# Kernel tuning notes

Measured on AMD Instinct MI355X. Metric: run time of the kernel, lower is better.

Reference implementation:

```python
import jax, jax.numpy as jnp
import numpy as np

D = 1024
H = 8  # num_heads hardcoded in module
B = 16384


def setup_inputs() -> dict:
    key = jax.random.key(0)
    ks = jax.random.split(key, 12)
    s = 0.02
    return {
        "text_feat": jax.random.normal(ks[0], (B, D), jnp.float32),
        "image_feat": jax.random.normal(ks[1], (B, D), jnp.float32),
        # fuse_proj (nn.Linear): y = x @ W.T + b
        "fuse_w": jax.random.normal(ks[2], (D, D), jnp.float32) * s,
        "fuse_b": jax.random.normal(ks[3], (D,), jnp.float32) * s,
        # text_to_fused MHA params (torch packed in_proj layout: [Wq;Wk;Wv])
        "t_in_w": jax.random.normal(ks[4], (3 * D, D), jnp.float32) * s,
        "t_in_b": jax.random.normal(ks[5], (3 * D,), jnp.float32) * s,
        "t_out_w": jax.random.normal(ks[6], (D, D), jnp.float32) * s,
        "t_out_b": jax.random.normal(ks[7], (D,), jnp.float32) * s,
        # image_to_fused MHA params
        "i_in_w": jax.random.normal(ks[8], (3 * D, D), jnp.float32) * s,
        "i_in_b": jax.random.normal(ks[9], (3 * D,), jnp.float32) * s,
        "i_out_w": jax.random.normal(ks[10], (D, D), jnp.float32) * s,
        "i_out_b": jax.random.normal(ks[11], (D,), jnp.float32) * s,
    }


def _mha_len1(q_feat, kv_feat, in_w, in_b, out_w, out_b):
    """nn.MultiheadAttention with query/key/value of seq-len 1 (eval, no dropout)."""
    d = q_feat.shape[-1]
    dh = d // H
    wq, wk, wv = in_w[:d], in_w[d:2 * d], in_w[2 * d:]
    bq, bk, bv = in_b[:d], in_b[d:2 * d], in_b[2 * d:]
    q = (q_feat @ wq.T + bq).reshape(-1, H, dh)   # (B,H,dh)
    k = (kv_feat @ wk.T + bk).reshape(-1, H, dh)
    v = (kv_feat @ wv.T + bv).reshape(-1, H, dh)
    scores = jnp.sum(q * k, axis=-1) / jnp.sqrt(jnp.asarray(dh, q.dtype))  # (B,H)
    attn = jax.nn.softmax(scores[..., None], axis=-1)  # (B,H,1) -> all ones
    o = (attn * v).reshape(-1, d)                  # (B,D)
    return o @ out_w.T + out_b


def reference(text_feat, image_feat, fuse_w, fuse_b,
              t_in_w, t_in_b, t_out_w, t_out_b,
              i_in_w, i_in_b, i_out_w, i_out_b):
    fused = (text_feat + image_feat) @ fuse_w.T + fuse_b  # (B,D)
    out_text = _mha_len1(text_feat, fused, t_in_w, t_in_b, t_out_w, t_out_b)
    out_image = _mha_len1(image_feat, fused, i_in_w, i_in_b, i_out_w, i_out_b)
    return (out_text, out_image, fused)
```

## Files before the change

### kernel.cpp

```cpp
#include <hip/hip_runtime.h>
#include <stdint.h>

typedef float f32x4 __attribute__((ext_vector_type(4)));
typedef short s16x8 __attribute__((ext_vector_type(8)));
typedef short s16x4 __attribute__((ext_vector_type(4)));

__device__ __forceinline__ short f2bf(float f){
  union { float f; unsigned u; } v; v.f = f;
  unsigned r = v.u + 0x7FFFu + ((v.u >> 16) & 1u);
  return (short)(r >> 16);
}
__device__ __forceinline__ float bf2f(short h){
  union { unsigned u; float f; } v; v.u = ((unsigned)(unsigned short)h) << 16;
  return v.f;
}

__global__ void k_prep(const float* __restrict__ ta, const float* __restrict__ tb,
                       short* __restrict__ so,
                       const float* __restrict__ c0s, short* __restrict__ c0d,
                       const float* __restrict__ c1s, short* __restrict__ c1d,
                       const float* __restrict__ c2s, short* __restrict__ c2d,
                       const float* __restrict__ t0s, short* __restrict__ t0d,
                       const float* __restrict__ t1s, short* __restrict__ t1d,
                       const float* __restrict__ t2s, short* __restrict__ t2d,
                       const float* __restrict__ wt, const float* __restrict__ bvt, const float* __restrict__ obt,
                       const float* __restrict__ wi, const float* __restrict__ bvi, const float* __restrict__ obi,
                       float* __restrict__ bc){
  int bid = blockIdx.x;
  int tid = threadIdx.x;
  if (bid < 8192) {
    long i = (long)bid * 256 + tid;
    const f32x4* a4 = (const f32x4*)ta;
    const f32x4* b4 = (const f32x4*)tb;
    f32x4 x0 = a4[2*i], x1 = a4[2*i+1];
    f32x4 y0 = b4[2*i], y1 = b4[2*i+1];
    s16x8 r;
    #pragma unroll
    for (int j=0;j<4;j++){ r[j] = f2bf(x0[j]+y0[j]); r[j+4] = f2bf(x1[j]+y1[j]); }
    *(s16x8*)(so + i*8) = r;
    return;
  }
  bid -= 8192;
  if (bid < 3072) {
    int z = bid >> 10, b = bid & 1023;
    const float* in = (z==0) ? c0s : ((z==1) ? c1s : c2s);
    short* out      = (z==0) ? c0d : ((z==1) ? c1d : c2d);
    long i = (long)b*256 + tid;
    f32x4 v = ((const f32x4*)in)[i];
    s16x4 r;
    #pragma unroll
    for (int j=0;j<4;j++) r[j] = f2bf(v[j]);
    *(s16x4*)(out + i*4) = r;
  } else if (bid < 6144) {
    int q = bid - 3072;
    int z = q >> 10, b = q & 1023;
    const float* in = (z==0) ? t0s : ((z==1) ? t1s : t2s);
    short* out      = (z==0) ? t0d : ((z==1) ? t1d : t2d);
    __shared__ float tile[32][33];
    int tx = tid & 31, ty = tid >> 5;
    int c0 = (b & 31)*32, r0 = (b >> 5)*32;
    #pragma unroll
    for (int i=ty; i<32; i+=8)
      tile[i][tx] = in[(long)(r0+i)*1024 + c0 + tx];
    __syncthreads();
    #pragma unroll
    for (int i=ty; i<32; i+=8)
      out[(long)(c0+i)*1024 + r0 + tx] = f2bf(tile[tx][i]);
  } else {
    int q = bid - 6144;
    int z = q >> 8, b = q & 255;
    const float* w  = z ? wi  : wt;
    const float* bv = z ? bvi : bvt;
    const float* ob = z ? obi : obt;
    int n = b*4 + (tid>>6);
    int lane = tid & 63;
    const float* row = w + (long)n*1024;
    float acc = 0.f;
    for (int j=lane; j<1024; j+=64) acc += row[j]*bv[j];
    #pragma unroll
    for (int m=32;m;m>>=1) acc += __shfl_xor(acc, m, 64);
    if (lane==0) bc[z*1024+n] = acc + ob[n];
  }
}

#define GLDS(src, dst) __builtin_amdgcn_global_load_lds( \
    (const __attribute__((address_space(1))) void*)(src), \
    (__attribute__((address_space(3))) void*)(dst), 16, 0, 0)

__device__ __forceinline__
void gemm_small_body(const short* __restrict__ A, const short* __restrict__ B,
                     short* __restrict__ C, int N, int K, int m0, int n0,
                     short* ldsA, short* ldsB, int tid)
{
  const int lane = tid & 63;
  const int wv = tid >> 6;
  const int wm = wv >> 1, wn = wv & 1;

  f32x4 acc[4][4];
  #pragma unroll
  for (int i=0;i<4;i++)
    #pragma unroll
    for (int j=0;j<4;j++) acc[i][j] = (f32x4){0.f,0.f,0.f,0.f};

  const int bo0 = wv*1024 + lane*16;
  const int bo1 = bo0 + 4096;
  const int r0 = bo0 >> 6, c0 = bo0 & 63;
  const int r1 = bo1 >> 6, c1 = bo1 & 63;
  const long rsb = (long)K * 2;

  const char* Ab = (const char*)A;
  const char* Bb = (const char*)B;
  char* lA = (char*)ldsA;
  char* lB = (char*)ldsB;

  const int nkt = K >> 5;
  for (int kt = 0; kt < nkt; ++kt) {
    const long kb = (long)kt * 64;
    GLDS(Ab + (long)(m0 + r0)*rsb + kb + c0, lA + wv*1024);
    GLDS(Ab + (long)(m0 + r1)*rsb + kb + c1, lA + 4096 + wv*1024);
    GLDS(Bb + (long)(n0 + r0)*rsb + kb + c0, lB + wv*1024);
    GLDS(Bb + (long)(n0 + r1)*rsb + kb + c1, lB + 4096 + wv*1024);
    __syncthreads();

    s16x8 af[4], bfv[4];
    #pragma unroll
    for (int i=0;i<4;i++)
      af[i] = *(const s16x8*)(lA + (wm*64 + i*16 + (lane&15))*64 + (lane>>4)*16);
    #pragma unroll
    for (int j=0;j<4;j++)
      bfv[j] = *(const s16x8*)(lB + (wn*64 + j*16 + (lane&15))*64 + (lane>>4)*16);

    #pragma unroll
    for (int i=0;i<4;i++)
      #pragma unroll
      for (int j=0;j<4;j++)
        acc[i][j] = __builtin_amdgcn_mfma_f32_16x16x32_bf16(af[i], bfv[j], acc[i][j], 0, 0, 0);
    __syncthreads();
  }

  #pragma unroll
  for (int j=0;j<4;j++){
    int gn = n0 + wn*64 + j*16 + (lane&15);
    #pragma unroll
    for (int i=0;i<4;i++){
      int gmb = m0 + wm*64 + i*16 + ((lane>>4)*4);
      #pragma unroll
      for (int r=0;r<4;r++)
        C[(long)(gmb+r)*N + gn] = f2bf(acc[i][j][r]);
    }
  }
}

__global__ __launch_bounds__(256, 2)
void gemm_wc(const short* __restrict__ Abase, const short* __restrict__ Bbase,
             short* __restrict__ Cbase, long zA, long zB, long zC)
{
  __shared__ __align__(16) short ldsA[128*32];
  __shared__ __align__(16) short ldsB[128*32];
  gemm_small_body(Abase + (long)blockIdx.z*zA, Bbase + (long)blockIdx.z*zB,
                  Cbase + (long)blockIdx.z*zC, 1024, 1024,
                  blockIdx.x*128, blockIdx.y*128, ldsA, ldsB, threadIdx.x);
}

__global__ __launch_bounds__(256, 2)
void k_b2g2(const short* __restrict__ Wc, const float* __restrict__ fuse_b,
            const float* __restrict__ bc, float* __restrict__ b_all,
            const short* __restrict__ fuse_wT, short* __restrict__ W2)
{
  __shared__ __align__(16) short ldsA[128*32];
  __shared__ __align__(16) short ldsB[128*32];
  int bid = blockIdx.x;
  if (bid < 512) {
    int n = bid*4 + (threadIdx.x>>6);
    int lane = threadIdx.x & 63;
    const short* row = Wc + (long)n*1024;
    float acc = 0.f;
    for (int j=lane; j<1024; j+=64) acc += bf2f(row[j])*fuse_b[j];
    #pragma unroll
    for (int m=32;m;m>>=1) acc += __shfl_xor(acc, m, 64);
    if (lane==0) b_all[1024+n] = acc + bc[n];
    return;
  }
  if (bid < 516) {
    int i = (bid - 512)*256 + threadIdx.x;
    b_all[i] = fuse_b[i];
    return;
  }
  int g = bid - 516;
  gemm_small_body(Wc, fuse_wT, W2, 1024, 1024,
                  (g & 15)*128, (g >> 4)*128, ldsA, ldsB, threadIdx.x);
}

#define MFMA16 __builtin_amdgcn_mfma_f32_16x16x32_bf16
#define VMW4 asm volatile("s_waitcnt vmcnt(4)" ::: "memory")
#define VMW0 asm volatile("s_waitcnt vmcnt(0)" ::: "memory")
#define LGKM0 asm volatile("s_waitcnt lgkmcnt(0)" ::: "memory")
#define MEMF asm volatile("" ::: "memory")

__global__ __launch_bounds__(512, 2)
void gemm_main(const short* __restrict__ A, const short* __restrict__ B,
               float* __restrict__ O, const float* __restrict__ bias,
               int M, int N)
{
  __shared__ __align__(16) char lds[131072];
  constexpr int K = 1024;
  constexpr int nkt = 16;

  const int nbn = N >> 8;
  const int nwg = (M >> 8) * nbn;
  const int cpx = nwg >> 3;
  int bid = blockIdx.x;
  int swz = (bid & 7) * cpx + (bid >> 3);
  const int m0 = (swz / nbn) << 8;
  const int n0 = (swz % nbn) << 8;

  const int tid  = threadIdx.x;
  const int lane = tid & 63;
  const int wid  = tid >> 6;
  const int wm   = wid >> 2;
  const int wn   = wid & 3;
  const long rsb = (long)K * 2;

  f32x4 acc[8][4];
  #pragma unroll
  for (int i=0;i<8;i++)
    #pragma unroll
    for (int j=0;j<4;j++) acc[i][j] = (f32x4){0.f,0.f,0.f,0.f};

  const int lo0 = (((lane>>4)<<4)) ^ ((lane&7)<<4);
  const int lo1 = lo0 ^ 64;
  const char* pA0 = lds + wm*16384 + (lane&15)*128 + lo0;
  const char* pA1 = lds + wm*16384 + (lane&15)*128 + lo1;
  const char* pB0 = lds + 65536 + wn*8192 + (lane&15)*128 + lo0;
  const char* pB1 = lds + 65536 + wn*8192 + (lane&15)*128 + lo1;

  int sdst[2][2];
  const char* Apt[2][2];
  const char* Bpt[2][2];
  #pragma unroll
  for (int H=0;H<2;H++)
    #pragma unroll
    for (int sb=0;sb<2;sb++){
      int c = H*1024 + sb*512 + wid*64 + lane;
      int q = c ^ ((c>>3)&7);
      sdst[H][sb] = (H*1024 + sb*512 + wid*64) << 4;
      const long roff = (long)(q >> 3) * rsb + ((q & 7) << 4);
      Apt[H][sb] = (const char*)A + (long)m0*rsb + roff + 128;
      Bpt[H][sb] = (const char*)B + (long)n0*rsb + roff + 256;
    }

  #pragma unroll
  for (int H=0;H<2;H++)
    #pragma unroll
    for (int sb=0;sb<2;sb++)
      GLDS(Apt[H][sb] - 128, lds + sdst[H][sb]);
  #pragma unroll
  for (int H=0;H<2;H++)
    #pragma unroll
    for (int sb=0;sb<2;sb++)
      GLDS(Bpt[H][sb] - 256, lds + 65536 + sdst[H][sb]);
  #pragma unroll
  for (int H=0;H<2;H++)
    #pragma unroll
    for (int sb=0;sb<2;sb++)
      GLDS(Bpt[H][sb] - 128, lds + 98304 + sdst[H][sb]);
  VMW4; MEMF;
  __builtin_amdgcn_s_barrier();

  s16x8 bfr[4][2];
  s16x8 af[8];

  #pragma unroll
  for (int t = 0; t < nkt; ++t) {
    const int RB = (t & 1) << 15;
    #pragma unroll
    for (int j=0;j<4;j++){
      bfr[j][0] = *(const s16x8*)(pB0 + RB + j*2048);
      bfr[j][1] = *(const s16x8*)(pB1 + RB + j*2048);
    }
    #pragma unroll
    for (int i=0;i<8;i++) af[i] = *(const s16x8*)(pA0 + RB + i*2048);
    VMW4; MEMF;
    __builtin_amdgcn_s_barrier();
    if (t+1 < nkt) {
      const int AB2 = ((t+1)&1) << 15;
      #pragma unroll
      for (int H=0;H<2;H++)
        #pragma unroll
        for (int sb=0;sb<2;sb++){
          GLDS(Apt[H][sb], lds + AB2 + sdst[H][sb]);
          Apt[H][sb] += 128;
        }
    }
    LGKM0;
    __builtin_amdgcn_s_setprio(1);
    #pragma unroll
    for (int i=0;i<8;i++)
      #pragma unroll
      for (int j=0;j<4;j++)
        acc[i][j] = MFMA16(af[i], bfr[j][0], acc[i][j], 0, 0, 0);
    __builtin_amdgcn_s_setprio(0);
    #pragma unroll
    for (int i=0;i<8;i++) af[i] = *(const s16x8*)(pA1 + RB + i*2048);
    VMW0; MEMF;
    __builtin_amdgcn_s_barrier();
    if (t+2 < nkt) {
      const int BB2 = 65536 + RB;
      #pragma unroll
      for (int H=0;H<2;H++)
        #pragma unroll
        for (int sb=0;sb<2;sb++){
          GLDS(Bpt[H][sb], lds + BB2 + sdst[H][sb]);
          Bpt[H][sb] += 128;
        }
    }
    LGKM0;
    __builtin_amdgcn_s_setprio(1);
    #pragma unroll
    for (int i=0;i<8;i++)
      #pragma unroll
      for (int j=0;j<4;j++)
        acc[i][j] = MFMA16(af[i], bfr[j][1], acc[i][j], 0, 0, 0);
    __builtin_amdgcn_s_setprio(0);
  }

  const long BD = (long)M * 1024L;
  #pragma unroll
  for (int j=0;j<4;j++){
    int gn = n0 + wn*64 + j*16 + (lane&15);
    float bb = bias[gn];
    int region = gn >> 10;
    long rbase = (region==0) ? 2*BD : ((region==1) ? 0L : BD);
    int col = gn & 1023;
    #pragma unroll
    for (int i=0;i<8;i++){
      int gr = m0 + wm*128 + i*16 + ((lane>>4)<<2);
      #pragma unroll
      for (int r=0;r<4;r++)
        O[rbase + (long)(gr+r)*1024 + col] = acc[i][j][r] + bb;
    }
  }
}

extern "C" void kernel_launch(void* const* d_in, const int* in_sizes, int n_in,
                              void* d_out, int out_size, void* d_ws, size_t ws_size,
                              hipStream_t stream) {
  const float* text    = (const float*)d_in[0];
  const float* image   = (const float*)d_in[1];
  const float* fuse_w  = (const float*)d_in[2];
  const float* fuse_b  = (const float*)d_in[3];
  const float* t_in_w  = (const float*)d_in[4];
  const float* t_in_b  = (const float*)d_in[5];
  const float* t_out_w = (const float*)d_in[6];
  const float* t_out_b = (const float*)d_in[7];
  const float* i_in_w  = (const float*)d_in[8];
  const float* i_in_b  = (const float*)d_in[9];
  const float* i_out_w = (const float*)d_in[10];
  const float* i_out_b = (const float*)d_in[11];
  float* out = (float*)d_out;

  const long DD = 1024L*1024L;
  char* ws = (char*)d_ws;
  short* s_bf    = (short*)ws; ws += 16384L*1024*2;
  short* W_all   = (short*)ws; ws += 3*DD*2;
  short* wvT     = (short*)ws; ws += 2*DD*2;
  short* fuse_wT = (short*)ws; ws += DD*2;
  short* outw_st = (short*)ws; ws += 2*DD*2;
  short* Wc_st   = (short*)ws; ws += 2*DD*2;
  float* bc      = (float*)ws; ws += 2048*4;
  float* b_all   = (float*)ws; ws += 3072*4;

  k_prep<<<14848, 256, 0, stream>>>(text, image, s_bf,
                                    fuse_w, W_all,
                                    t_out_w, outw_st,
                                    i_out_w, outw_st + DD,
                                    t_in_w + 2*DD, wvT,
                                    i_in_w + 2*DD, wvT + DD,
                                    fuse_w, fuse_wT,
                                    t_out_w, t_in_b + 2048, t_out_b,
                                    i_out_w, i_in_b + 2048, i_out_b, bc);

  gemm_wc<<<dim3(8,8,2), 256, 0, stream>>>(outw_st, wvT, Wc_st, DD, DD, DD);

  k_b2g2<<<644, 256, 0, stream>>>(Wc_st, fuse_b, bc, b_all, fuse_wT, W_all + DD);

  gemm_main<<<dim3(768), 512, 0, stream>>>(s_bf, W_all, out, b_all, 16384, 3072);
}
```

Baseline: 209.5 us.

## Spread activation add-convert blocks across prep and small weight-GEMM kernels

The bandwidth-bound text+image add and bf16 conversion, previously done entirely in the prep kernel, is now split into three slices. The slices run as extra blocks appended to the prep kernel, the Wc GEMM kernel and the bias/W2 kernel. This lets the low-occupancy small GEMMs (128 blocks, 644 blocks) share the GPU with streaming work instead of leaving compute units idle. It adds block-index dispatch logic and risks memory contention slowing the small GEMMs on the critical path.

After: 195.7 us. 1.07x faster.

```diff
diff --git a/kernel.cpp b/kernel.cpp
--- a/kernel.cpp
+++ b/kernel.cpp
@@ -15,32 +15,34 @@
   return v.f;
 }
 
-__global__ void k_prep(const float* __restrict__ ta, const float* __restrict__ tb,
-                       short* __restrict__ so,
-                       const float* __restrict__ c0s, short* __restrict__ c0d,
-                       const float* __restrict__ c1s, short* __restrict__ c1d,
-                       const float* __restrict__ c2s, short* __restrict__ c2d,
-                       const float* __restrict__ t0s, short* __restrict__ t0d,
-                       const float* __restrict__ t1s, short* __restrict__ t1d,
-                       const float* __restrict__ t2s, short* __restrict__ t2d,
-                       const float* __restrict__ wt, const float* __restrict__ bvt, const float* __restrict__ obt,
-                       const float* __restrict__ wi, const float* __restrict__ bvi, const float* __restrict__ obi,
-                       float* __restrict__ bc){
+__device__ __forceinline__
+void addcvt_block(int gbid, int tid, const float* __restrict__ ta,
+                  const float* __restrict__ tb, short* __restrict__ so){
+  long i = (long)gbid * 256 + tid;
+  const f32x4* a4 = (const f32x4*)ta;
+  const f32x4* b4 = (const f32x4*)tb;
+  f32x4 x0 = a4[2*i], x1 = a4[2*i+1];
+  f32x4 y0 = b4[2*i], y1 = b4[2*i+1];
+  s16x8 r;
+  #pragma unroll
+  for (int j=0;j<4;j++){ r[j] = f2bf(x0[j]+y0[j]); r[j+4] = f2bf(x1[j]+y1[j]); }
+  *(s16x8*)(so + i*8) = r;
+}
+
+__global__ void k_prep1(const float* __restrict__ ta, const float* __restrict__ tb,
+                        short* __restrict__ so,
+                        const float* __restrict__ c0s, short* __restrict__ c0d,
+                        const float* __restrict__ c1s, short* __restrict__ c1d,
+                        const float* __restrict__ c2s, short* __restrict__ c2d,
+                        const float* __restrict__ t0s, short* __restrict__ t0d,
+                        const float* __restrict__ t1s, short* __restrict__ t1d,
+                        const float* __restrict__ t2s, short* __restrict__ t2d,
+                        const float* __restrict__ wt, const float* __restrict__ bvt, const float* __restrict__ obt,
+                        const float* __restrict__ wi, const float* __restrict__ bvi, const float* __restrict__ obi,
+                        float* __restrict__ bc){
   int bid = blockIdx.x;
   int tid = threadIdx.x;
-  if (bid < 8192) {
-    long i = (long)bid * 256 + tid;
-    const f32x4* a4 = (const f32x4*)ta;
-    const f32x4* b4 = (const f32x4*)tb;
-    f32x4 x0 = a4[2*i], x1 = a4[2*i+1];
-    f32x4 y0 = b4[2*i], y1 = b4[2*i+1];
-    s16x8 r;
-    #pragma unroll
-    for (int j=0;j<4;j++){ r[j] = f2bf(x0[j]+y0[j]); r[j+4] = f2bf(x1[j]+y1[j]); }
-    *(s16x8*)(so + i*8) = r;
-    return;
-  }
-  bid -= 8192;
+  if (bid >= 6656) { addcvt_block(bid - 6656, tid, ta, tb, so); return; }
   if (bid < 3072) {
     int z = bid >> 10, b = bid & 1023;
     const float* in = (z==0) ? c0s : ((z==1) ? c1s : c2s);
@@ -152,24 +154,31 @@
 }
 
 __global__ __launch_bounds__(256, 2)
-void gemm_wc(const short* __restrict__ Abase, const short* __restrict__ Bbase,
-             short* __restrict__ Cbase, long zA, long zB, long zC)
-{
-  __shared__ __align__(16) short ldsA[128*32];
-  __shared__ __align__(16) short ldsB[128*32];
-  gemm_small_body(Abase + (long)blockIdx.z*zA, Bbase + (long)blockIdx.z*zB,
-                  Cbase + (long)blockIdx.z*zC, 1024, 1024,
-                  blockIdx.x*128, blockIdx.y*128, ldsA, ldsB, threadIdx.x);
-}
-
-__global__ __launch_bounds__(256, 2)
-void k_b2g2(const short* __restrict__ Wc, const float* __restrict__ fuse_b,
-            const float* __restrict__ bc, float* __restrict__ b_all,
-            const short* __restrict__ fuse_wT, short* __restrict__ W2)
+void k_wc_add(const short* __restrict__ Abase, const short* __restrict__ Bbase,
+              short* __restrict__ Cbase, long zA, long zB, long zC,
+              const float* __restrict__ ta, const float* __restrict__ tb,
+              short* __restrict__ so)
 {
   __shared__ __align__(16) short ldsA[128*32];
   __shared__ __align__(16) short ldsB[128*32];
   int bid = blockIdx.x;
+  if (bid >= 128) { addcvt_block(2600 + bid - 128, threadIdx.x, ta, tb, so); return; }
+  int z = bid >> 6, y = (bid >> 3) & 7, x = bid & 7;
+  gemm_small_body(Abase + (long)z*zA, Bbase + (long)z*zB, Cbase + (long)z*zC,
+                  1024, 1024, x*128, y*128, ldsA, ldsB, threadIdx.x);
+}
+
+__global__ __launch_bounds__(256, 2)
+void k_b2g2(const short* __restrict__ Wc, const float* __restrict__ fuse_b,
+            const float* __restrict__ bc, float* __restrict__ b_all,
+            const short* __restrict__ fuse_wT, short* __restrict__ W2,
+            const float* __restrict__ ta, const float* __restrict__ tb,
+            short* __restrict__ so)
+{
+  __shared__ __align__(16) short ldsA[128*32];
+  __shared__ __align__(16) short ldsB[128*32];
+  int bid = blockIdx.x;
+  if (bid >= 644) { addcvt_block(5600 + bid - 644, threadIdx.x, ta, tb, so); return; }
   if (bid < 512) {
     int n = bid*4 + (threadIdx.x>>6);
     int lane = threadIdx.x & 63;
@@ -370,7 +379,7 @@
   float* bc      = (float*)ws; ws += 2048*4;
   float* b_all   = (float*)ws; ws += 3072*4;
 
-  k_prep<<<14848, 256, 0, stream>>>(text, image, s_bf,
+  k_prep1<<<9256, 256, 0, stream>>>(text, image, s_bf,
                                     fuse_w, W_all,
                                     t_out_w, outw_st,
                                     i_out_w, outw_st + DD,
@@ -380,9 +389,11 @@
                                     t_out_w, t_in_b + 2048, t_out_b,
                                     i_out_w, i_in_b + 2048, i_out_b, bc);
 
-  gemm_wc<<<dim3(8,8,2), 256, 0, stream>>>(outw_st, wvT, Wc_st, DD, DD, DD);
-
-  k_b2g2<<<644, 256, 0, stream>>>(Wc_st, fuse_b, bc, b_all, fuse_wT, W_all + DD);
+  k_wc_add<<<3128, 256, 0, stream>>>(outw_st, wvT, Wc_st, DD, DD, DD,
+                                     text, image, s_bf);
+
+  k_b2g2<<<3236, 256, 0, stream>>>(Wc_st, fuse_b, bc, b_all, fuse_wT, W_all + DD,
+                                   text, image, s_bf);
 
   gemm_main<<<dim3(768), 512, 0, stream>>>(s_bf, W_all, out, b_all, 16384, 3072);
 }
```
